# Optimization experiments

Measured on AMD Instinct MI355X. Metric: run time of the kernel, lower is better.

The kernel has to match this reference:

```python
import jax, jax.numpy as jnp
import numpy as np


def setup_inputs() -> dict:
    key = jax.random.key(0)
    kq, kk, kv = jax.random.split(key, 3)
    B, H, T, D = 1, 16, 4096, 64
    Q = jax.random.normal(kq, (B, H, T, D), dtype=jnp.float32)
    K = jax.random.normal(kk, (B, H, T, D), dtype=jnp.float32)
    V = jax.random.normal(kv, (B, H, T, D), dtype=jnp.float32)
    return {"Q": Q, "K": K, "V": V}


def reference(Q, K, V):
    B, H, T, D = Q.shape
    # ALiBi slopes: m_h = 2^(-8*h/H), h = 1..H (deterministic buffer)
    slopes = jnp.exp2(-8.0 * jnp.arange(1, H + 1, dtype=jnp.float32) / H)
    pos = jnp.arange(T, dtype=jnp.float32)
    dist = jnp.abs(pos[None, :] - pos[:, None])          # (T, T)
    bias = slopes[:, None, None] * dist                   # (H, T, T)
    scale = jnp.sqrt(jnp.asarray(D, dtype=Q.dtype))
    scores = jnp.einsum('bhtd,bhsd->bhts', Q, K) / scale - bias[None]
    attn = jax.nn.softmax(scores, axis=-1)
    return jnp.einsum('bhts,bhsd->bhtd', attn, V)
```

## Files before the change

kernel.cpp:

```cpp
#include <hip/hip_runtime.h>
#include <hip/hip_bf16.h>
#include <stdint.h>

typedef float f4    __attribute__((ext_vector_type(4)));
typedef float f32x4 __attribute__((ext_vector_type(4)));
typedef short s16x8 __attribute__((ext_vector_type(8)));
typedef short s16x4 __attribute__((ext_vector_type(4)));
typedef unsigned short u16;

#define T_LEN 4096
#define NHEAD 16
#define DHEAD 64
#define KVBLK 64
#define NT    (T_LEN / KVBLK)

#if __has_builtin(__builtin_amdgcn_exp2f)
#define EXP2(x) __builtin_amdgcn_exp2f(x)
#else
#define EXP2(x) exp2f(x)
#endif

#define SLOT_F 4160
#define NSLOTS 1728
#define CONV_BYTES (16u * 4096u * 64u * 2u * 2u)
#define CHUNK_BYTES ((size_t)CONV_BYTES + (size_t)NSLOTS * SLOT_F * 4u)

__device__ __forceinline__ uint32_t pk2(float a, float b){
  uint32_t ua = __builtin_bit_cast(uint32_t, a) + 0x8000u;
  uint32_t ub = __builtin_bit_cast(uint32_t, b) + 0x8000u;
  return __builtin_amdgcn_perm(ub, ua, 0x07060302u);
}
__device__ __forceinline__ int swk(int r){ return (r ^ (r >> 3)) & 7; }
__device__ __forceinline__ int sw(int r){ return swk(r) << 3; }
__device__ __forceinline__ int slotbase(int h){
  return (h <= 9) ? (h - 8) * 128 : (h == 10 ? 256 : 448 + (h - 11) * 256);
}

__global__ __launch_bounds__(256)
void cvt_k(const float* __restrict__ K, u16* __restrict__ Kb){
  const size_t i = ((size_t)blockIdx.x * 256 + threadIdx.x) * 8;
  f4 a = *(const f4*)(K + i);
  f4 b = *(const f4*)(K + i + 4);
  union { uint32_t w[4]; s16x8 v; } u;
  u.w[0] = pk2(a[0], a[1]); u.w[1] = pk2(a[2], a[3]);
  u.w[2] = pk2(b[0], b[1]); u.w[3] = pk2(b[2], b[3]);
  *(s16x8*)(Kb + i) = u.v;
}

__global__ __launch_bounds__(256)
void cvt_vt(const float* __restrict__ V, u16* __restrict__ VT){
  __shared__ u16 tile[64][66];
  const int h  = blockIdx.x >> 6;
  const int kt = blockIdx.x & 63;
  const int t  = threadIdx.x;
  const float* Vh = V + ((size_t)h * T_LEN + kt * 64) * DHEAD;

  const int r = t >> 2, c = (t & 3) * 16;
  f4 x0 = *(const f4*)(Vh + r*64 + c);
  f4 x1 = *(const f4*)(Vh + r*64 + c + 4);
  f4 x2 = *(const f4*)(Vh + r*64 + c + 8);
  f4 x3 = *(const f4*)(Vh + r*64 + c + 12);
  uint32_t* tp = (uint32_t*)&tile[r][c];
  tp[0] = pk2(x0[0],x0[1]); tp[1] = pk2(x0[2],x0[3]);
  tp[2] = pk2(x1[0],x1[1]); tp[3] = pk2(x1[2],x1[3]);
  tp[4] = pk2(x2[0],x2[1]); tp[5] = pk2(x2[2],x2[3]);
  tp[6] = pk2(x3[0],x3[1]); tp[7] = pk2(x3[2],x3[3]);
  __syncthreads();

  const int d = t >> 2, ks = (t & 3) * 16;
  u16* op = VT + ((size_t)h * DHEAD + d) * T_LEN + kt * 64 + ks;
  union { uint32_t w[4]; s16x8 v; } o0, o1;
#pragma unroll
  for (int q = 0; q < 4; ++q)
    o0.w[q] = (uint32_t)tile[ks + 2*q][d]     | ((uint32_t)tile[ks + 2*q + 1][d] << 16);
#pragma unroll
  for (int q = 0; q < 4; ++q)
    o1.w[q] = (uint32_t)tile[ks + 8 + 2*q][d] | ((uint32_t)tile[ks + 9 + 2*q][d] << 16);
  *(s16x8*)(op)     = o0.v;
  *(s16x8*)(op + 8) = o1.v;
}

__global__ __launch_bounds__(256, 4)
void alibi_attn5(const float* __restrict__ Qg,
                 const u16* __restrict__ Kb,
                 const u16* __restrict__ VTb,
                 float* __restrict__ Og,
                 float* __restrict__ part)
{
  __shared__ u16 kbuf[2][KVBLK * DHEAD];
  __shared__ u16 vbuf[2][DHEAD * KVBLK];

  const int bid = blockIdx.x;
  int h, qt, c, n;
  if (bid < 1280){
    h = 11 + (bid >> 8); int r = bid & 255; qt = r >> 2; c = r & 3; n = 4;
  } else if (bid < 1472){
    int r = bid - 1280; h = 10; qt = r / 3; c = r - qt * 3; n = 3;
  } else if (bid < 1728){
    int r = bid - 1472; h = 8 + (r >> 7); r &= 127; qt = r >> 1; c = r & 1; n = 2;
  } else {
    int r = bid - 1728; h = r >> 6; qt = r & 63; c = 0; n = 1;
  }

  const int tid  = threadIdx.x;
  const int wv   = tid >> 6;
  const int lane = tid & 63;
  const int lg   = lane >> 4;
  const int ln   = lane & 15;

  const int q0   = qt * 64;
  const int qrow = q0 + wv * 16 + ln;
  const float slope = exp2f(-0.5f * (float)(h + 1));
  const float cs = 0.125f * 1.44269504089f;
  const float bs = slope * 1.44269504089f;
  const size_t headoff = (size_t)h * T_LEN * DHEAD;

  const int Di = (int)(36.0f / bs);
  int lo = (q0 - Di) >> 6;           if (lo < 0) lo = 0;
  int hi = (q0 + 63 + Di) >> 6;      if (hi > NT - 1) hi = NT - 1;
  const int len = hi - lo + 1;
  const int start = lo + (c * len) / n;
  const int end   = lo + ((c + 1) * len) / n;

  s16x8 qf0, qf1;
  {
    const float* qp = Qg + headoff + (size_t)qrow * DHEAD + lg * 8;
    f4 x = *(const f4*)qp;        f4 y = *(const f4*)(qp + 4);
    f4 z = *(const f4*)(qp + 32); f4 v = *(const f4*)(qp + 36);
    union { uint32_t w_[4]; s16x8 v_; } u0, u1;
    u0.w_[0] = pk2(x[0]*cs, x[1]*cs); u0.w_[1] = pk2(x[2]*cs, x[3]*cs);
    u0.w_[2] = pk2(y[0]*cs, y[1]*cs); u0.w_[3] = pk2(y[2]*cs, y[3]*cs);
    u1.w_[0] = pk2(z[0]*cs, z[1]*cs); u1.w_[1] = pk2(z[2]*cs, z[3]*cs);
    u1.w_[2] = pk2(v[0]*cs, v[1]*cs); u1.w_[3] = pk2(v[2]*cs, v[3]*cs);
    qf0 = u0.v_; qf1 = u1.v_;
  }

  f32x4 acc[4];
#pragma unroll
  for (int dt = 0; dt < 4; ++dt) acc[dt] = (f32x4)(0.0f);
  float lsum = 0.0f;
  const float base0 = (float)qrow - (float)(lg * 4);

  int koffs[4][2];
#pragma unroll
  for (int kt = 0; kt < 4; ++kt){
    const int key = kt*16 + ln, sz = sw(key);
    koffs[kt][0] = (((key*64      + lg*8) ^ sz)) * 2;
    koffs[kt][1] = (((key*64 + 32 + lg*8) ^ sz)) * 2;
  }
  int voffs[4][4];
#pragma unroll
  for (int dt = 0; dt < 4; ++dt){
    const int d = dt*16 + ln, sz = sw(d);
#pragma unroll
    for (int kt = 0; kt < 4; ++kt)
      voffs[dt][kt] = (((d*64 + kt*16 + lg*4) ^ sz)) * 2;
  }

  const u16* Kh = Kb  + headoff;
  const u16* Vh = VTb + headoff;
  const int sA = wv * 128 + lane;
  const int sB = sA + 64;
  const int keyA = sA >> 3, gA = (sA & 7) ^ swk(keyA);
  const int keyB = sB >> 3, gB = (sB & 7) ^ swk(keyB);
  const int kidxA = keyA * 64 + gA * 8;
  const int kidxB = keyB * 64 + gB * 8;
  const int vidxA = keyA * T_LEN + gA * 8;
  const int vidxB = keyB * T_LEN + gB * 8;
  const int dstA = sA * 16, dstB = sB * 16;

  s16x8 rkA, rkB, rvA, rvB;
  auto ldregs = [&](int t){
    const u16* kp = Kh + (size_t)t * (KVBLK * DHEAD);
    const u16* vp = Vh + (size_t)t * KVBLK;
    rkA = *(const s16x8*)(kp + kidxA);  rkB = *(const s16x8*)(kp + kidxB);
    rvA = *(const s16x8*)(vp + vidxA);  rvB = *(const s16x8*)(vp + vidxB);
  };
  auto wrregs = [&](u16* kb_, u16* vb_){
    *(s16x8*)((char*)kb_ + dstA) = rkA;  *(s16x8*)((char*)kb_ + dstB) = rkB;
    *(s16x8*)((char*)vb_ + dstA) = rvA;  *(s16x8*)((char*)vb_ + dstB) = rvB;
  };

  auto compute = [&](const u16* kb_, const u16* vb_, int kv){
    f32x4 S[4];
    __builtin_amdgcn_s_setprio(1);
#pragma unroll
    for (int kt = 0; kt < 4; ++kt){
      s16x8 k0 = *(const s16x8*)((const char*)kb_ + koffs[kt][0]);
      s16x8 k1 = *(const s16x8*)((const char*)kb_ + koffs[kt][1]);
      f32x4 cc = (f32x4)(0.0f);
      cc = __builtin_amdgcn_mfma_f32_16x16x32_bf16(k0, qf0, cc, 0, 0, 0);
      cc = __builtin_amdgcn_mfma_f32_16x16x32_bf16(k1, qf1, cc, 0, 0, 0);
      S[kt] = cc;
    }
    __builtin_amdgcn_s_setprio(0);

    const float bi = base0 - (float)(kv * KVBLK);
    float p[16];
#pragma unroll
    for (int kt = 0; kt < 4; ++kt)
#pragma unroll
      for (int r = 0; r < 4; ++r)
        p[kt*4 + r] = EXP2(fmaf(-bs, fabsf(bi - (float)(kt*16 + r)), S[kt][r]));

    lsum += (((p[0]+p[1]) + (p[2]+p[3])) + ((p[4]+p[5]) + (p[6]+p[7])))
          + (((p[8]+p[9]) + (p[10]+p[11])) + ((p[12]+p[13]) + (p[14]+p[15])));

    s16x4 pb[4];
#pragma unroll
    for (int kt = 0; kt < 4; ++kt){
      union { uint32_t w_[2]; s16x4 v_; } u;
      u.w_[0] = pk2(p[kt*4+0], p[kt*4+1]);
      u.w_[1] = pk2(p[kt*4+2], p[kt*4+3]);
      pb[kt] = u.v_;
    }

    __builtin_amdgcn_s_setprio(1);
#pragma unroll
    for (int dt = 0; dt < 4; ++dt){
#pragma unroll
      for (int kt = 0; kt < 4; ++kt){
        const s16x4 vf = *(const s16x4*)((const char*)vb_ + voffs[dt][kt]);
        acc[dt] = __builtin_amdgcn_mfma_f32_16x16x16bf16_1k(vf, pb[kt], acc[dt], 0, 0, 0);
      }
    }
    __builtin_amdgcn_s_setprio(0);
  };

  if (start < end){
    ldregs(start);
    wrregs(kbuf[0], vbuf[0]);
    __syncthreads();

    const int hi_i = end - 1;
    int t = start;
#pragma unroll 1
    while (t + 1 < hi_i){
      ldregs(t + 1);
      compute(kbuf[0], vbuf[0], t);
      wrregs(kbuf[1], vbuf[1]);
      __syncthreads();
      ldregs(t + 2);
      compute(kbuf[1], vbuf[1], t + 1);
      wrregs(kbuf[0], vbuf[0]);
      __syncthreads();
      t += 2;
    }
    if (t < hi_i){
      ldregs(t + 1);
      compute(kbuf[0], vbuf[0], t);
      wrregs(kbuf[1], vbuf[1]);
      __syncthreads();
      compute(kbuf[1], vbuf[1], t + 1);
    } else {
      compute(kbuf[0], vbuf[0], t);
    }
  }

  lsum += __shfl_xor(lsum, 16, 64);
  lsum += __shfl_xor(lsum, 32, 64);

  if (n == 1){
    const float inv = 1.0f / lsum;
    float* op = Og + headoff + (size_t)qrow * DHEAD + lg * 4;
#pragma unroll
    for (int dt = 0; dt < 4; ++dt){
      f4 o;
      o[0] = acc[dt][0] * inv; o[1] = acc[dt][1] * inv;
      o[2] = acc[dt][2] * inv; o[3] = acc[dt][3] * inv;
      *(f4*)(op + dt*16) = o;
    }
  } else {
    float* slot = part + (size_t)(slotbase(h) + qt * n + c) * SLOT_F;
    const int row = wv * 16 + ln;
    float* op = slot + row * 64 + lg * 4;
#pragma unroll
    for (int dt = 0; dt < 4; ++dt)
      *(f4*)(op + dt*16) = acc[dt];
    if (lg == 0) slot[4096 + row] = lsum;
  }
}

__global__ __launch_bounds__(256)
void combine_k(const float* __restrict__ part, float* __restrict__ Og){
  const int h  = 8 + (blockIdx.x >> 6);
  const int qt = blockIdx.x & 63;
  const int n  = (h <= 9) ? 2 : (h == 10 ? 3 : 4);
  const int sb = slotbase(h) + qt * n;

  const int t   = threadIdx.x;
  const int row = t >> 2;
  const int seg = (t & 3) * 16;

  f4 a0 = (f4)(0.0f), a1 = (f4)(0.0f), a2 = (f4)(0.0f), a3 = (f4)(0.0f);
  float l = 0.0f;
#pragma unroll 1
  for (int c = 0; c < n; ++c){
    const float* sp = part + (size_t)(sb + c) * SLOT_F;
    const float* rp = sp + row * 64 + seg;
    a0 += *(const f4*)(rp);
    a1 += *(const f4*)(rp + 4);
    a2 += *(const f4*)(rp + 8);
    a3 += *(const f4*)(rp + 12);
    l  += sp[4096 + row];
  }
  const float inv = 1.0f / l;
  float* op = Og + (((size_t)h * T_LEN + qt * 64 + row) * DHEAD) + seg;
  f4 o0, o1, o2, o3;
  o0[0]=a0[0]*inv; o0[1]=a0[1]*inv; o0[2]=a0[2]*inv; o0[3]=a0[3]*inv;
  o1[0]=a1[0]*inv; o1[1]=a1[1]*inv; o1[2]=a1[2]*inv; o1[3]=a1[3]*inv;
  o2[0]=a2[0]*inv; o2[1]=a2[1]*inv; o2[2]=a2[2]*inv; o2[3]=a2[3]*inv;
  o3[0]=a3[0]*inv; o3[1]=a3[1]*inv; o3[2]=a3[2]*inv; o3[3]=a3[3]*inv;
  *(f4*)(op)      = o0;
  *(f4*)(op + 4)  = o1;
  *(f4*)(op + 8)  = o2;
  *(f4*)(op + 12) = o3;
}

__global__ __launch_bounds__(256, 4)
void alibi_attn4(const float* __restrict__ Qg,
                 const u16* __restrict__ Kb,
                 const u16* __restrict__ VTb,
                 float* __restrict__ Og)
{
  __shared__ u16 kbuf[2][KVBLK * DHEAD];
  __shared__ u16 vbuf[2][DHEAD * KVBLK];

  const int bid = blockIdx.x;
  const int fid = (bid & 7) * 128 + (bid >> 3);
  const int h  = fid & 15;
  const int qt = fid >> 4;

  const int tid  = threadIdx.x;
  const int wv   = tid >> 6;
  const int lane = tid & 63;
  const int lg   = lane >> 4;
  const int ln   = lane & 15;

  const int q0   = qt * 64;
  const int qrow = q0 + wv * 16 + ln;
  const float slope = exp2f(-0.5f * (float)(h + 1));
  const float cs = 0.125f * 1.44269504089f;
  const float bs = slope * 1.44269504089f;
  const size_t headoff = (size_t)h * T_LEN * DHEAD;

  const int Di = (int)(36.0f / bs);
  int lo = (q0 - Di) >> 6;           if (lo < 0) lo = 0;
  int hi = (q0 + 63 + Di) >> 6;      if (hi > NT - 1) hi = NT - 1;

  s16x8 qf0, qf1;
  {
    const float* qp = Qg + headoff + (size_t)qrow * DHEAD + lg * 8;
    f4 x = *(const f4*)qp;        f4 y = *(const f4*)(qp + 4);
    f4 z = *(const f4*)(qp + 32); f4 v = *(const f4*)(qp + 36);
    union { uint32_t w_[4]; s16x8 v_; } u0, u1;
    u0.w_[0] = pk2(x[0]*cs, x[1]*cs); u0.w_[1] = pk2(x[2]*cs, x[3]*cs);
    u0.w_[2] = pk2(y[0]*cs, y[1]*cs); u0.w_[3] = pk2(y[2]*cs, y[3]*cs);
    u1.w_[0] = pk2(z[0]*cs, z[1]*cs); u1.w_[1] = pk2(z[2]*cs, z[3]*cs);
    u1.w_[2] = pk2(v[0]*cs, v[1]*cs); u1.w_[3] = pk2(v[2]*cs, v[3]*cs);
    qf0 = u0.v_; qf1 = u1.v_;
  }

  f32x4 acc[4];
#pragma unroll
  for (int dt = 0; dt < 4; ++dt) acc[dt] = (f32x4)(0.0f);
  float lsum = 0.0f;
  const float base0 = (float)qrow - (float)(lg * 4);

  int koffs[4][2];
#pragma unroll
  for (int kt = 0; kt < 4; ++kt){
    const int key = kt*16 + ln, sz = sw(key);
    koffs[kt][0] = (((key*64      + lg*8) ^ sz)) * 2;
    koffs[kt][1] = (((key*64 + 32 + lg*8) ^ sz)) * 2;
  }
  int voffs[4][4];
#pragma unroll
  for (int dt = 0; dt < 4; ++dt){
    const int d = dt*16 + ln, sz = sw(d);
#pragma unroll
    for (int kt = 0; kt < 4; ++kt)
      voffs[dt][kt] = (((d*64 + kt*16 + lg*4) ^ sz)) * 2;
  }

  const u16* Kh = Kb  + headoff;
  const u16* Vh = VTb + headoff;
  const int sA = wv * 128 + lane;
  const int sB = sA + 64;
  const int keyA = sA >> 3, gA = (sA & 7) ^ swk(keyA);
  const int keyB = sB >> 3, gB = (sB & 7) ^ swk(keyB);
  const int kidxA = keyA * 64 + gA * 8;
  const int kidxB = keyB * 64 + gB * 8;
  const int vidxA = keyA * T_LEN + gA * 8;
  const int vidxB = keyB * T_LEN + gB * 8;
  const int dstA = sA * 16, dstB = sB * 16;

  s16x8 rkA, rkB, rvA, rvB;
  auto ldregs = [&](int t){
    const u16* kp = Kh + (size_t)t * (KVBLK * DHEAD);
    const u16* vp = Vh + (size_t)t * KVBLK;
    rkA = *(const s16x8*)(kp + kidxA);  rkB = *(const s16x8*)(kp + kidxB);
    rvA = *(const s16x8*)(vp + vidxA);  rvB = *(const s16x8*)(vp + vidxB);
  };
  auto wrregs = [&](u16* kb_, u16* vb_){
    *(s16x8*)((char*)kb_ + dstA) = rkA;  *(s16x8*)((char*)kb_ + dstB) = rkB;
    *(s16x8*)((char*)vb_ + dstA) = rvA;  *(s16x8*)((char*)vb_ + dstB) = rvB;
  };

  auto compute = [&](const u16* kb_, const u16* vb_, int kv){
    f32x4 S[4];
    __builtin_amdgcn_s_setprio(1);
#pragma unroll
    for (int kt = 0; kt < 4; ++kt){
      s16x8 k0 = *(const s16x8*)((const char*)kb_ + koffs[kt][0]);
      s16x8 k1 = *(const s16x8*)((const char*)kb_ + koffs[kt][1]);
      f32x4 cc = (f32x4)(0.0f);
      cc = __builtin_amdgcn_mfma_f32_16x16x32_bf16(k0, qf0, cc, 0, 0, 0);
      cc = __builtin_amdgcn_mfma_f32_16x16x32_bf16(k1, qf1, cc, 0, 0, 0);
      S[kt] = cc;
    }
    __builtin_amdgcn_s_setprio(0);

    const float bi = base0 - (float)(kv * KVBLK);
    float p[16];
#pragma unroll
    for (int kt = 0; kt < 4; ++kt)
#pragma unroll
      for (int r = 0; r < 4; ++r)
        p[kt*4 + r] = EXP2(fmaf(-bs, fabsf(bi - (float)(kt*16 + r)), S[kt][r]));

    lsum += (((p[0]+p[1]) + (p[2]+p[3])) + ((p[4]+p[5]) + (p[6]+p[7])))
          + (((p[8]+p[9]) + (p[10]+p[11])) + ((p[12]+p[13]) + (p[14]+p[15])));

    s16x4 pb[4];
#pragma unroll
    for (int kt = 0; kt < 4; ++kt){
      union { uint32_t w_[2]; s16x4 v_; } u;
      u.w_[0] = pk2(p[kt*4+0], p[kt*4+1]);
      u.w_[1] = pk2(p[kt*4+2], p[kt*4+3]);
      pb[kt] = u.v_;
    }

    __builtin_amdgcn_s_setprio(1);
#pragma unroll
    for (int dt = 0; dt < 4; ++dt){
#pragma unroll
      for (int kt = 0; kt < 4; ++kt){
        const s16x4 vf = *(const s16x4*)((const char*)vb_ + voffs[dt][kt]);
        acc[dt] = __builtin_amdgcn_mfma_f32_16x16x16bf16_1k(vf, pb[kt], acc[dt], 0, 0, 0);
      }
    }
    __builtin_amdgcn_s_setprio(0);
  };

  ldregs(lo);
  wrregs(kbuf[0], vbuf[0]);
  __syncthreads();

  int t = lo;
#pragma unroll 1
  while (t + 1 < hi){
    ldregs(t + 1);
    compute(kbuf[0], vbuf[0], t);
    wrregs(kbuf[1], vbuf[1]);
    __syncthreads();
    ldregs(t + 2);
    compute(kbuf[1], vbuf[1], t + 1);
    wrregs(kbuf[0], vbuf[0]);
    __syncthreads();
    t += 2;
  }
  if (t < hi){
    ldregs(t + 1);
    compute(kbuf[0], vbuf[0], t);
    wrregs(kbuf[1], vbuf[1]);
    __syncthreads();
    compute(kbuf[1], vbuf[1], t + 1);
  } else {
    compute(kbuf[0], vbuf[0], t);
  }

  lsum += __shfl_xor(lsum, 16, 64);
  lsum += __shfl_xor(lsum, 32, 64);
  const float inv = 1.0f / lsum;
  float* op = Og + headoff + (size_t)qrow * DHEAD + lg * 4;
#pragma unroll
  for (int dt = 0; dt < 4; ++dt){
    f4 o;
    o[0] = acc[dt][0] * inv; o[1] = acc[dt][1] * inv;
    o[2] = acc[dt][2] * inv; o[3] = acc[dt][3] * inv;
    *(f4*)(op + dt*16) = o;
  }
}

__global__ __launch_bounds__(256, 2)
void alibi_attn_fb(const float* __restrict__ Qg,
                   const float* __restrict__ Kg,
                   const float* __restrict__ Vg,
                   float* __restrict__ Og)
{
  __shared__ u16 kbuf[2][KVBLK * DHEAD];
  __shared__ u16 vbuf[2][DHEAD * KVBLK];

  const int bid = blockIdx.x;
  const int fid = (bid & 7) * 64 + (bid >> 3);
  const int h  = fid >> 5;
  const int qt = fid & 31;

  const int tid  = threadIdx.x;
  const int wave = tid >> 6;
  const int lane = tid & 63;
  const int lg   = lane >> 4;
  const int ln   = lane & 15;

  const int qb = qt * 128 + wave * 32;
  const float slope = exp2f(-0.5f * (float)(h + 1));
  const float cs = 0.125f * 1.44269504089f;
  const float bs = slope * 1.44269504089f;
  const size_t headoff = (size_t)h * T_LEN * DHEAD;

  s16x8 qf[2][2];
#pragma unroll
  for (int rg = 0; rg < 2; ++rg)
#pragma unroll
    for (int dh = 0; dh < 2; ++dh){
      const float* qp = Qg + headoff + (size_t)(qb + rg*16 + ln) * DHEAD + dh*32 + lg*8;
      f4 x = *(const f4*)qp;
      f4 y = *(const f4*)(qp + 4);
      union { uint32_t w[4]; s16x8 v; } u;
      u.w[0] = pk2(x[0]*cs, x[1]*cs);
      u.w[1] = pk2(x[2]*cs, x[3]*cs);
      u.w[2] = pk2(y[0]*cs, y[1]*cs);
      u.w[3] = pk2(y[2]*cs, y[3]*cs);
      qf[rg][dh] = u.v;
    }

  f32x4 acc[2][4];
#pragma unroll
  for (int rg = 0; rg < 2; ++rg)
#pragma unroll
    for (int dt = 0; dt < 4; ++dt) acc[rg][dt] = (f32x4)(0.0f);
  float mreg[2] = {-1e30f, -1e30f};
  float lreg[2] = {0.0f, 0.0f};
  const float qposf[2] = {(float)(qb + ln), (float)(qb + 16 + ln)};
  const float koffb = (float)(lg * 4);

  f4 st4[8];
  const int vk0  = (tid >> 2) * 2;
  const int vseg = (tid & 3) * 16;
  const int krow = (tid - 128) >> 1;
  const int kseg = ((tid - 128) & 1) * 32;
  const float* Vb = Vg + headoff;
  const float* Kb_ = Kg + headoff;

  auto stage_load = [&](int kv){
    const int kb = kv * KVBLK;
    if (tid < 128){
      const float* vp = Vb + (size_t)(kb + vk0) * DHEAD + vseg;
      st4[0] = *(const f4*)(vp);      st4[1] = *(const f4*)(vp + 4);
      st4[2] = *(const f4*)(vp + 8);  st4[3] = *(const f4*)(vp + 12);
      st4[4] = *(const f4*)(vp + 64); st4[5] = *(const f4*)(vp + 68);
      st4[6] = *(const f4*)(vp + 72); st4[7] = *(const f4*)(vp + 76);
    } else {
      const float* kp = Kb_ + (size_t)(kb + krow) * DHEAD + kseg;
#pragma unroll
      for (int j = 0; j < 8; ++j) st4[j] = *(const f4*)(kp + j*4);
    }
  };
  auto stage_store = [&](int b){
    if (tid < 128){
#pragma unroll
      for (int i = 0; i < 16; ++i){
        const int d = vseg + i;
        uint32_t pr = pk2(st4[i>>2][i&3], st4[4 + (i>>2)][i&3]);
        *(uint32_t*)&vbuf[b][(d*64 + vk0) ^ sw(d)] = pr;
      }
    } else {
#pragma unroll
      for (int i = 0; i < 4; ++i){
        union { uint32_t w[4]; s16x8 v; } u;
        u.w[0] = pk2(st4[i*2][0],   st4[i*2][1]);
        u.w[1] = pk2(st4[i*2][2],   st4[i*2][3]);
        u.w[2] = pk2(st4[i*2+1][0], st4[i*2+1][1]);
        u.w[3] = pk2(st4[i*2+1][2], st4[i*2+1][3]);
        *(s16x8*)&kbuf[b][(krow*64 + kseg + i*8) ^ sw(krow)] = u.v;
      }
    }
  };

  stage_load(0);
  stage_store(0);
  __syncthreads();
  int cur = 0;

#pragma unroll 1
  for (int kv = 0; kv < NT; ++kv){
    if (kv + 1 < NT) stage_load(kv + 1);

    const float kbf = (float)(kv * KVBLK);
    const u16* kb_ = kbuf[cur];
    const u16* vb_ = vbuf[cur];

    s16x8 kf[4][2];
#pragma unroll
    for (int kt = 0; kt < 4; ++kt){
      const int key = kt*16 + ln;
      const int sz  = sw(key);
      kf[kt][0] = *(const s16x8*)&kb_[(key*64 +      lg*8) ^ sz];
      kf[kt][1] = *(const s16x8*)&kb_[(key*64 + 32 + lg*8) ^ sz];
    }
    f32x4 S[2][4];
#pragma unroll
    for (int rg = 0; rg < 2; ++rg)
#pragma unroll
      for (int kt = 0; kt < 4; ++kt){
        f32x4 c = (f32x4)(0.0f);
        c = __builtin_amdgcn_mfma_f32_16x16x32_bf16(kf[kt][0], qf[rg][0], c, 0, 0, 0);
        c = __builtin_amdgcn_mfma_f32_16x16x32_bf16(kf[kt][1], qf[rg][1], c, 0, 0, 0);
        S[rg][kt] = c;
      }

    s16x4 pb[2][4];
#pragma unroll
    for (int rg = 0; rg < 2; ++rg){
      const float base = qposf[rg] - kbf - koffb;
#pragma unroll
      for (int kt = 0; kt < 4; ++kt)
#pragma unroll
        for (int r = 0; r < 4; ++r)
          S[rg][kt][r] = fmaf(-bs, fabsf(base - (float)(kt*16 + r)), S[rg][kt][r]);

      float a0 = fmaxf(fmaxf(S[rg][0][0], S[rg][0][1]), fmaxf(S[rg][0][2], S[rg][0][3]));
      float a1 = fmaxf(fmaxf(S[rg][1][0], S[rg][1][1]), fmaxf(S[rg][1][2], S[rg][1][3]));
      float a2 = fmaxf(fmaxf(S[rg][2][0], S[rg][2][1]), fmaxf(S[rg][2][2], S[rg][2][3]));
      float a3 = fmaxf(fmaxf(S[rg][3][0], S[rg][3][1]), fmaxf(S[rg][3][2], S[rg][3][3]));
      float mx = fmaxf(fmaxf(a0, a1), fmaxf(a2, a3));
      mx = fmaxf(mx, __shfl_xor(mx, 16, 64));
      mx = fmaxf(mx, __shfl_xor(mx, 32, 64));

      const float mo = mreg[rg];
      const float mn = fmaxf(mo, mx);
      const float scl = EXP2(mo - mn);
      mreg[rg] = mn;

      float p[16];
#pragma unroll
      for (int kt = 0; kt < 4; ++kt)
#pragma unroll
        for (int r = 0; r < 4; ++r)
          p[kt*4 + r] = EXP2(S[rg][kt][r] - mn);

      float s0 = (p[0]+p[1]) + (p[2]+p[3]);
      float s1 = (p[4]+p[5]) + (p[6]+p[7]);
      float s2 = (p[8]+p[9]) + (p[10]+p[11]);
      float s3 = (p[12]+p[13]) + (p[14]+p[15]);
      float sum = (s0+s1) + (s2+s3);
      sum += __shfl_xor(sum, 16, 64);
      sum += __shfl_xor(sum, 32, 64);
      lreg[rg] = lreg[rg] * scl + sum;

#pragma unroll
      for (int dt = 0; dt < 4; ++dt) acc[rg][dt] *= scl;

#pragma unroll
      for (int kt = 0; kt < 4; ++kt){
        union { uint32_t w[2]; s16x4 v; } u;
        u.w[0] = pk2(p[kt*4+0], p[kt*4+1]);
        u.w[1] = pk2(p[kt*4+2], p[kt*4+3]);
        pb[rg][kt] = u.v;
      }
    }

#pragma unroll
    for (int dt = 0; dt < 4; ++dt){
      const int d  = dt*16 + ln;
      const int sz = sw(d);
#pragma unroll
      for (int kt = 0; kt < 4; ++kt){
        const s16x4 vf = *(const s16x4*)&vb_[(d*64 + kt*16 + lg*4) ^ sz];
        acc[0][dt] = __builtin_amdgcn_mfma_f32_16x16x16bf16_1k(vf, pb[0][kt], acc[0][dt], 0, 0, 0);
        acc[1][dt] = __builtin_amdgcn_mfma_f32_16x16x16bf16_1k(vf, pb[1][kt], acc[1][dt], 0, 0, 0);
      }
    }

    if (kv + 1 < NT){
      stage_store(cur ^ 1);
      __syncthreads();
      cur ^= 1;
    }
  }

#pragma unroll
  for (int rg = 0; rg < 2; ++rg){
    const float inv = 1.0f / lreg[rg];
    float* op = Og + headoff + (size_t)(qb + rg*16 + ln) * DHEAD + lg*4;
#pragma unroll
    for (int dt = 0; dt < 4; ++dt){
      f4 o;
      o[0] = acc[rg][dt][0] * inv;
      o[1] = acc[rg][dt][1] * inv;
      o[2] = acc[rg][dt][2] * inv;
      o[3] = acc[rg][dt][3] * inv;
      *(f4*)(op + dt*16) = o;
    }
  }
}

extern "C" void kernel_launch(void* const* d_in, const int* in_sizes, int n_in,
                              void* d_out, int out_size, void* d_ws, size_t ws_size,
                              hipStream_t stream)
{
  const float* Q = (const float*)d_in[0];
  const float* K = (const float*)d_in[1];
  const float* V = (const float*)d_in[2];
  float* O = (float*)d_out;

  if (ws_size >= CHUNK_BYTES){
    u16* Kb = (u16*)d_ws;
    u16* VT = Kb + (size_t)NHEAD * T_LEN * DHEAD;
    float* part = (float*)((char*)d_ws + CONV_BYTES);
    hipLaunchKernelGGL(cvt_k,  dim3(2048), dim3(256), 0, stream, K, Kb);
    hipLaunchKernelGGL(cvt_vt, dim3(1024), dim3(256), 0, stream, V, VT);
    hipLaunchKernelGGL(alibi_attn5, dim3(2240), dim3(256), 0, stream, Q, Kb, VT, O, part);
    hipLaunchKernelGGL(combine_k, dim3(512), dim3(256), 0, stream, part, O);
  } else if (ws_size >= CONV_BYTES){
    u16* Kb = (u16*)d_ws;
    u16* VT = Kb + (size_t)NHEAD * T_LEN * DHEAD;
    hipLaunchKernelGGL(cvt_k,  dim3(2048), dim3(256), 0, stream, K, Kb);
    hipLaunchKernelGGL(cvt_vt, dim3(1024), dim3(256), 0, stream, V, VT);
    hipLaunchKernelGGL(alibi_attn4, dim3(1024), dim3(256), 0, stream, Q, Kb, VT, O);
  } else {
    hipLaunchKernelGGL(alibi_attn_fb, dim3(512), dim3(256), 0, stream, Q, K, V, O);
  }
}
```

Measured before the change: 81.60 us.

## Merge K/V conversion kernels and split heads 12-15 into five KV chunks

Fuses the K-convert and V-transpose kernels into a single launch, which removes one kernel launch. The attention kernel is templated on the number of KV chunks used for the widest-window heads (12-15), and it uses 5 chunks when the workspace is large enough. Launch bounds are raised to 5 waves per SIMD. Together these aim to balance the per-block work across heads and improve occupancy, at the cost of more partial slots for the combine step to read and a tighter register budget.

```diff
diff --git a/kernel.cpp b/kernel.cpp
--- a/kernel.cpp
+++ b/kernel.cpp
@@ -21,9 +21,8 @@
 #endif
 
 #define SLOT_F 4160
-#define NSLOTS 1728
 #define CONV_BYTES (16u * 4096u * 64u * 2u * 2u)
-#define CHUNK_BYTES ((size_t)CONV_BYTES + (size_t)NSLOTS * SLOT_F * 4u)
+#define CHUNK_BYTES(NCB) ((size_t)CONV_BYTES + (size_t)(704 + 256*(NCB)) * SLOT_F * 4u)
 
 __device__ __forceinline__ uint32_t pk2(float a, float b){
   uint32_t ua = __builtin_bit_cast(uint32_t, a) + 0x8000u;
@@ -32,55 +31,57 @@
 }
 __device__ __forceinline__ int swk(int r){ return (r ^ (r >> 3)) & 7; }
 __device__ __forceinline__ int sw(int r){ return swk(r) << 3; }
-__device__ __forceinline__ int slotbase(int h){
-  return (h <= 9) ? (h - 8) * 128 : (h == 10 ? 256 : 448 + (h - 11) * 256);
+__device__ __forceinline__ int slotbase(int h, int ncb){
+  return (h <= 9) ? (h - 8) * 128 : (h == 10 ? 256 : (h == 11 ? 448 : 704 + (h - 12) * 64 * ncb));
 }
 
 __global__ __launch_bounds__(256)
-void cvt_k(const float* __restrict__ K, u16* __restrict__ Kb){
-  const size_t i = ((size_t)blockIdx.x * 256 + threadIdx.x) * 8;
-  f4 a = *(const f4*)(K + i);
-  f4 b = *(const f4*)(K + i + 4);
-  union { uint32_t w[4]; s16x8 v; } u;
-  u.w[0] = pk2(a[0], a[1]); u.w[1] = pk2(a[2], a[3]);
-  u.w[2] = pk2(b[0], b[1]); u.w[3] = pk2(b[2], b[3]);
-  *(s16x8*)(Kb + i) = u.v;
+void cvt_kv(const float* __restrict__ K, const float* __restrict__ V,
+            u16* __restrict__ Kb, u16* __restrict__ VT){
+  __shared__ u16 tile[64][66];
+  if (blockIdx.x < 2048){
+    const size_t i = ((size_t)blockIdx.x * 256 + threadIdx.x) * 8;
+    f4 a = *(const f4*)(K + i);
+    f4 b = *(const f4*)(K + i + 4);
+    union { uint32_t w[4]; s16x8 v; } u;
+    u.w[0] = pk2(a[0], a[1]); u.w[1] = pk2(a[2], a[3]);
+    u.w[2] = pk2(b[0], b[1]); u.w[3] = pk2(b[2], b[3]);
+    *(s16x8*)(Kb + i) = u.v;
+  } else {
+    const int vb = blockIdx.x - 2048;
+    const int h  = vb >> 6;
+    const int kt = vb & 63;
+    const int t  = threadIdx.x;
+    const float* Vh = V + ((size_t)h * T_LEN + kt * 64) * DHEAD;
+
+    const int r = t >> 2, c = (t & 3) * 16;
+    f4 x0 = *(const f4*)(Vh + r*64 + c);
+    f4 x1 = *(const f4*)(Vh + r*64 + c + 4);
+    f4 x2 = *(const f4*)(Vh + r*64 + c + 8);
+    f4 x3 = *(const f4*)(Vh + r*64 + c + 12);
+    uint32_t* tp = (uint32_t*)&tile[r][c];
+    tp[0] = pk2(x0[0],x0[1]); tp[1] = pk2(x0[2],x0[3]);
+    tp[2] = pk2(x1[0],x1[1]); tp[3] = pk2(x1[2],x1[3]);
+    tp[4] = pk2(x2[0],x2[1]); tp[5] = pk2(x2[2],x2[3]);
+    tp[6] = pk2(x3[0],x3[1]); tp[7] = pk2(x3[2],x3[3]);
+    __syncthreads();
+
+    const int d = t >> 2, ks = (t & 3) * 16;
+    u16* op = VT + ((size_t)h * DHEAD + d) * T_LEN + kt * 64 + ks;
+    union { uint32_t w[4]; s16x8 v; } o0, o1;
+#pragma unroll
+    for (int q = 0; q < 4; ++q)
+      o0.w[q] = (uint32_t)tile[ks + 2*q][d]     | ((uint32_t)tile[ks + 2*q + 1][d] << 16);
+#pragma unroll
+    for (int q = 0; q < 4; ++q)
+      o1.w[q] = (uint32_t)tile[ks + 8 + 2*q][d] | ((uint32_t)tile[ks + 9 + 2*q][d] << 16);
+    *(s16x8*)(op)     = o0.v;
+    *(s16x8*)(op + 8) = o1.v;
+  }
 }
 
-__global__ __launch_bounds__(256)
-void cvt_vt(const float* __restrict__ V, u16* __restrict__ VT){
-  __shared__ u16 tile[64][66];
-  const int h  = blockIdx.x >> 6;
-  const int kt = blockIdx.x & 63;
-  const int t  = threadIdx.x;
-  const float* Vh = V + ((size_t)h * T_LEN + kt * 64) * DHEAD;
-
-  const int r = t >> 2, c = (t & 3) * 16;
-  f4 x0 = *(const f4*)(Vh + r*64 + c);
-  f4 x1 = *(const f4*)(Vh + r*64 + c + 4);
-  f4 x2 = *(const f4*)(Vh + r*64 + c + 8);
-  f4 x3 = *(const f4*)(Vh + r*64 + c + 12);
-  uint32_t* tp = (uint32_t*)&tile[r][c];
-  tp[0] = pk2(x0[0],x0[1]); tp[1] = pk2(x0[2],x0[3]);
-  tp[2] = pk2(x1[0],x1[1]); tp[3] = pk2(x1[2],x1[3]);
-  tp[4] = pk2(x2[0],x2[1]); tp[5] = pk2(x2[2],x2[3]);
-  tp[6] = pk2(x3[0],x3[1]); tp[7] = pk2(x3[2],x3[3]);
-  __syncthreads();
-
-  const int d = t >> 2, ks = (t & 3) * 16;
-  u16* op = VT + ((size_t)h * DHEAD + d) * T_LEN + kt * 64 + ks;
-  union { uint32_t w[4]; s16x8 v; } o0, o1;
-#pragma unroll
-  for (int q = 0; q < 4; ++q)
-    o0.w[q] = (uint32_t)tile[ks + 2*q][d]     | ((uint32_t)tile[ks + 2*q + 1][d] << 16);
-#pragma unroll
-  for (int q = 0; q < 4; ++q)
-    o1.w[q] = (uint32_t)tile[ks + 8 + 2*q][d] | ((uint32_t)tile[ks + 9 + 2*q][d] << 16);
-  *(s16x8*)(op)     = o0.v;
-  *(s16x8*)(op + 8) = o1.v;
-}
-
-__global__ __launch_bounds__(256, 4)
+template<int NCB>
+__global__ __launch_bounds__(256, 5)
 void alibi_attn5(const float* __restrict__ Qg,
                  const u16* __restrict__ Kb,
                  const u16* __restrict__ VTb,
@@ -91,15 +92,18 @@
   __shared__ u16 vbuf[2][DHEAD * KVBLK];
 
   const int bid = blockIdx.x;
+  constexpr int B12 = 256 * NCB;
   int h, qt, c, n;
-  if (bid < 1280){
-    h = 11 + (bid >> 8); int r = bid & 255; qt = r >> 2; c = r & 3; n = 4;
-  } else if (bid < 1472){
-    int r = bid - 1280; h = 10; qt = r / 3; c = r - qt * 3; n = 3;
-  } else if (bid < 1728){
-    int r = bid - 1472; h = 8 + (r >> 7); r &= 127; qt = r >> 1; c = r & 1; n = 2;
+  if (bid < B12){
+    h = 12 + bid / (64 * NCB); int r = bid % (64 * NCB); qt = r / NCB; c = r % NCB; n = NCB;
+  } else if (bid < B12 + 256){
+    int r = bid - B12; h = 11; qt = r >> 2; c = r & 3; n = 4;
+  } else if (bid < B12 + 448){
+    int r = bid - B12 - 256; h = 10; qt = r / 3; c = r - qt * 3; n = 3;
+  } else if (bid < B12 + 704){
+    int r = bid - B12 - 448; h = 8 + (r >> 7); r &= 127; qt = r >> 1; c = r & 1; n = 2;
   } else {
-    int r = bid - 1728; h = r >> 6; qt = r & 63; c = 0; n = 1;
+    int r = bid - B12 - 704; h = r >> 6; qt = r & 63; c = 0; n = 1;
   }
 
   const int tid  = threadIdx.x;
@@ -271,7 +275,7 @@
       *(f4*)(op + dt*16) = o;
     }
   } else {
-    float* slot = part + (size_t)(slotbase(h) + qt * n + c) * SLOT_F;
+    float* slot = part + (size_t)(slotbase(h, NCB) + qt * n + c) * SLOT_F;
     const int row = wv * 16 + ln;
     float* op = slot + row * 64 + lg * 4;
 #pragma unroll
@@ -281,12 +285,13 @@
   }
 }
 
+template<int NCB>
 __global__ __launch_bounds__(256)
 void combine_k(const float* __restrict__ part, float* __restrict__ Og){
   const int h  = 8 + (blockIdx.x >> 6);
   const int qt = blockIdx.x & 63;
-  const int n  = (h <= 9) ? 2 : (h == 10 ? 3 : 4);
-  const int sb = slotbase(h) + qt * n;
+  const int n  = (h <= 9) ? 2 : (h == 10 ? 3 : (h == 11 ? 4 : NCB));
+  const int sb = slotbase(h, NCB) + qt * n;
 
   const int t   = threadIdx.x;
   const int row = t >> 2;
@@ -715,20 +720,22 @@
   const float* V = (const float*)d_in[2];
   float* O = (float*)d_out;
 
-  if (ws_size >= CHUNK_BYTES){
+  if (ws_size >= CONV_BYTES){
     u16* Kb = (u16*)d_ws;
     u16* VT = Kb + (size_t)NHEAD * T_LEN * DHEAD;
-    float* part = (float*)((char*)d_ws + CONV_BYTES);
-    hipLaunchKernelGGL(cvt_k,  dim3(2048), dim3(256), 0, stream, K, Kb);
-    hipLaunchKernelGGL(cvt_vt, dim3(1024), dim3(256), 0, stream, V, VT);
-    hipLaunchKernelGGL(alibi_attn5, dim3(2240), dim3(256), 0, stream, Q, Kb, VT, O, part);
-    hipLaunchKernelGGL(combine_k, dim3(512), dim3(256), 0, stream, part, O);
-  } else if (ws_size >= CONV_BYTES){
-    u16* Kb = (u16*)d_ws;
-    u16* VT = Kb + (size_t)NHEAD * T_LEN * DHEAD;
-    hipLaunchKernelGGL(cvt_k,  dim3(2048), dim3(256), 0, stream, K, Kb);
-    hipLaunchKernelGGL(cvt_vt, dim3(1024), dim3(256), 0, stream, V, VT);
-    hipLaunchKernelGGL(alibi_attn4, dim3(1024), dim3(256), 0, stream, Q, Kb, VT, O);
+    hipLaunchKernelGGL(cvt_kv, dim3(3072), dim3(256), 0, stream, K, V, Kb, VT);
+
+    if (ws_size >= CHUNK_BYTES(5)){
+      float* part = (float*)((char*)d_ws + CONV_BYTES);
+      hipLaunchKernelGGL((alibi_attn5<5>), dim3(1216 + 256*5), dim3(256), 0, stream, Q, Kb, VT, O, part);
+      hipLaunchKernelGGL((combine_k<5>), dim3(512), dim3(256), 0, stream, part, O);
+    } else if (ws_size >= CHUNK_BYTES(4)){
+      float* part = (float*)((char*)d_ws + CONV_BYTES);
+      hipLaunchKernelGGL((alibi_attn5<4>), dim3(1216 + 256*4), dim3(256), 0, stream, Q, Kb, VT, O, part);
+      hipLaunchKernelGGL((combine_k<4>), dim3(512), dim3(256), 0, stream, part, O);
+    } else {
+      hipLaunchKernelGGL(alibi_attn4, dim3(1024), dim3(256), 0, stream, Q, Kb, VT, O);
+    }
   } else {
     hipLaunchKernelGGL(alibi_attn_fb, dim3(512), dim3(256), 0, stream, Q, K, V, O);
   }
```

Result: slower. 267.6 us (+227.9%).
